# Performance work log

Hardware: AMD Instinct MI355X
Metric: run time of the kernel (lower is better)

Reference implementation:

```python
import jax, jax.numpy as jnp
import numpy as np

N_STEPS = 10
DT = 0.01
TAU = 0.1
LAM = 0.1


def setup_inputs() -> dict:
    key = jax.random.key(0)
    k1, k2 = jax.random.split(key)
    x = jax.random.normal(k1, (4, 2048, 1024), dtype=jnp.float32)
    W = jax.random.normal(k2, (1024, 4096), dtype=jnp.float32) * 0.02
    return {"x": x, "W": W}


def reference(x, W):
    orig_shape = x.shape
    D = orig_shape[-1]
    x_flat = x.reshape(-1, D)                      # [N, d_model]
    b = x_flat @ W                                 # [N, d_lca]
    G = W.T @ W                                    # [d_lca, d_lca]
    G = G - jnp.diag(jnp.diag(G))                  # zero self-inhibition
    u0 = jnp.zeros_like(b)

    def step(u, _):
        a = jax.nn.relu(u - LAM)
        du = (b - a @ G - u) / TAU
        return u + DT * du, None

    u, _ = jax.lax.scan(step, u0, None, length=N_STEPS)
    a = jax.nn.relu(u - LAM)
    out = a @ W.T                                  # [N, d_model]
    return out.reshape(orig_shape)
```

## Files before the change

### kernel.cpp

```cpp
#include <hip/hip_runtime.h>
#include <hip/hip_bf16.h>


typedef __bf16 bf16_t;
typedef __bf16 bf16x8 __attribute__((ext_vector_type(8)));
typedef __bf16 bf16x4 __attribute__((ext_vector_type(4)));
typedef float  f32x4  __attribute__((ext_vector_type(4)));

__device__ __forceinline__ void g2lds16(const void* g, void* l) {
    __builtin_amdgcn_global_load_lds(
        (const __attribute__((address_space(1))) void*)g,
        (__attribute__((address_space(3))) void*)l,
        16, 0, 0);
}

template<int N> __device__ __forceinline__ void waitv() {
    if constexpr (N == 0) asm volatile("s_waitcnt vmcnt(0)" ::: "memory");
    else if constexpr (N == 1) asm volatile("s_waitcnt vmcnt(1)" ::: "memory");
    else if constexpr (N == 2) asm volatile("s_waitcnt vmcnt(2)" ::: "memory");
    else if constexpr (N == 3) asm volatile("s_waitcnt vmcnt(3)" ::: "memory");
    else if constexpr (N == 4) asm volatile("s_waitcnt vmcnt(4)" ::: "memory");
    else if constexpr (N == 5) asm volatile("s_waitcnt vmcnt(5)" ::: "memory");
    else if constexpr (N == 6) asm volatile("s_waitcnt vmcnt(6)" ::: "memory");
}
__device__ __forceinline__ void bar() { __builtin_amdgcn_s_barrier(); }
__device__ __forceinline__ void waitlgkm0() {
    asm volatile("s_waitcnt lgkmcnt(0)" ::: "memory");
}
__device__ __forceinline__ void fence() { asm volatile("" ::: "memory"); }

template<int n> struct IC { static constexpr int v = n; };

enum { MODE_B = 0, MODE_T = 1, MODE_STEP2 = 2, MODE_OUT = 3 };

template<int MODE, int BM>
__global__ __launch_bounds__(512, 2)
void gemm_bt(const bf16_t* __restrict__ A, const bf16_t* __restrict__ Bt,
             int N, int K,
             float*  __restrict__ outF,
             bf16_t* __restrict__ outH,
             bf16_t* __restrict__ bb,
             bf16_t* __restrict__ u,
             const float* __restrict__ g)
{
    constexpr int BN  = 256;
    constexpr int FM  = BM / 32;
    constexpr int FMH = FM / 2;
    constexpr int ASZ = BM * 128;
    constexpr int BSZ = BN * 128;

    __shared__ __attribute__((aligned(16))) bf16_t As[2 * BM * 64];
    __shared__ __attribute__((aligned(16))) bf16_t Bs[2 * BN * 64];

    const int t = threadIdx.x;
    const int l = t & 63;
    const int w = t >> 6;
    const int wm = (w >> 2) * (BM / 4);
    const int wn = (w & 3) * 32;

    const int gx  = gridDim.x;
    const int nwg = gx * gridDim.y;
    const int bid = blockIdx.y * gx + blockIdx.x;
    const int sw  = (bid & 7) * (nwg >> 3) + (bid >> 3);
    const int rowA = (sw / gx) * BM;
    const int colB = (sw % gx) * BN;

    const int srow = t >> 3;
    const int scol = (((t & 7) ^ (srow & 7)) << 3);
    const bf16_t* gB = Bt + (size_t)(colB + srow) * K + scol;
    char* sB = (char*)Bs + t * 16;
    auto stB = [&](int slot, int kt, int uu) {
        g2lds16(gB + (size_t)uu * 64 * K + kt * 64, sB + slot * BSZ + uu * 8192);
    };

    const int lrow = l & 15;
    const int c0 = ((l >> 4) << 4) ^ ((l & 7) << 4);
    const char* cAs = (const char*)As;
    const char* cBs = (const char*)Bs;
    auto rdA = [&](int slot, int qi, int ii, int p) {
        return (const bf16x8*)(cAs + slot * ASZ
            + (size_t)(qi * (BM / 2) + wm + ii * 16 + lrow) * 128 + (c0 ^ (p << 6)));
    };
    auto rdB = [&](int slot, int qj, int jj, int p) {
        return (const bf16x8*)(cBs + slot * BSZ
            + (size_t)(qj * 128 + wn + jj * 16 + lrow) * 128 + (c0 ^ (p << 6)));
    };

    f32x4 acc[FM][4];
#pragma unroll
    for (int i = 0; i < FM; ++i)
#pragma unroll
        for (int j = 0; j < 4; ++j)
#pragma unroll
            for (int r = 0; r < 4; ++r) acc[i][j][r] = 0.f;

    const int NT = K >> 6;

    if constexpr (BM == 256) {
        const bf16_t* gA = A + (size_t)(rowA + srow) * K + scol;
        char* sA = (char*)As + t * 16;
        auto stA = [&](int slot, int kt, int uu) {
            g2lds16(gA + (size_t)uu * 64 * K + kt * 64, sA + slot * ASZ + uu * 8192);
        };

        auto tile = [&](auto W0, auto W1, auto W2, int slot, int ktN, bool st) {
            const int ns = slot ^ 1;
            bf16x8 af[FMH][2], bf0[2][2], bf1[2][2];
            if (st) { stB(ns, ktN, 0); stB(ns, ktN, 1); }
            waitv<decltype(W0)::v>(); bar();
#pragma unroll
            for (int ii = 0; ii < FMH; ++ii)
#pragma unroll
                for (int p = 0; p < 2; ++p) af[ii][p] = *rdA(slot, 0, ii, p);
#pragma unroll
            for (int jj = 0; jj < 2; ++jj)
#pragma unroll
                for (int p = 0; p < 2; ++p) bf0[jj][p] = *rdB(slot, 0, jj, p);
            __builtin_amdgcn_s_setprio(1);
#pragma unroll
            for (int ii = 0; ii < FMH; ++ii)
#pragma unroll
                for (int jj = 0; jj < 2; ++jj)
#pragma unroll
                    for (int p = 0; p < 2; ++p)
                        acc[ii][jj] = __builtin_amdgcn_mfma_f32_16x16x32_bf16(
                            bf0[jj][p], af[ii][p], acc[ii][jj], 0, 0, 0);
            __builtin_amdgcn_s_setprio(0);
            if (st) { stA(ns, ktN, 0); stA(ns, ktN, 1); }
            waitv<decltype(W1)::v>(); bar();
#pragma unroll
            for (int jj = 0; jj < 2; ++jj)
#pragma unroll
                for (int p = 0; p < 2; ++p) bf1[jj][p] = *rdB(slot, 1, jj, p);
            __builtin_amdgcn_s_setprio(1);
#pragma unroll
            for (int ii = 0; ii < FMH; ++ii)
#pragma unroll
                for (int jj = 0; jj < 2; ++jj)
#pragma unroll
                    for (int p = 0; p < 2; ++p)
                        acc[ii][2 + jj] = __builtin_amdgcn_mfma_f32_16x16x32_bf16(
                            bf1[jj][p], af[ii][p], acc[ii][2 + jj], 0, 0, 0);
            __builtin_amdgcn_s_setprio(0);
            if (st) { stB(ns, ktN, 2); stB(ns, ktN, 3); }
            waitv<decltype(W2)::v>(); bar();
#pragma unroll
            for (int ii = 0; ii < FMH; ++ii)
#pragma unroll
                for (int p = 0; p < 2; ++p) af[ii][p] = *rdA(slot, 1, ii, p);
            __builtin_amdgcn_s_setprio(1);
#pragma unroll
            for (int ii = 0; ii < FMH; ++ii)
#pragma unroll
                for (int jj = 0; jj < 2; ++jj)
#pragma unroll
                    for (int p = 0; p < 2; ++p)
                        acc[FMH + ii][2 + jj] = __builtin_amdgcn_mfma_f32_16x16x32_bf16(
                            bf1[jj][p], af[ii][p], acc[FMH + ii][2 + jj], 0, 0, 0);
            __builtin_amdgcn_s_setprio(0);
            if (st) { stA(ns, ktN, 2); stA(ns, ktN, 3); }
            __builtin_amdgcn_s_setprio(1);
#pragma unroll
            for (int ii = 0; ii < FMH; ++ii)
#pragma unroll
                for (int jj = 0; jj < 2; ++jj)
#pragma unroll
                    for (int p = 0; p < 2; ++p)
                        acc[FMH + ii][jj] = __builtin_amdgcn_mfma_f32_16x16x32_bf16(
                            bf0[jj][p], af[ii][p], acc[FMH + ii][jj], 0, 0, 0);
            __builtin_amdgcn_s_setprio(0);
        };

        stB(0, 0, 0); stB(0, 0, 1);
        stA(0, 0, 0); stA(0, 0, 1);
        stB(0, 0, 2); stB(0, 0, 3);
        stA(0, 0, 2); stA(0, 0, 3);

        for (int kt = 0; kt < NT - 1; ++kt)
            tile(IC<6>{}, IC<6>{}, IC<6>{}, kt & 1, kt + 1, true);
        tile(IC<4>{}, IC<2>{}, IC<0>{}, (NT - 1) & 1, 0, false);
    } else {
        const int s_arow = t >> 3;
        const int s_acb  = ((t & 7) << 4) ^ ((s_arow & 7) << 4);
        const bf16_t* gAr = A + (size_t)(rowA + s_arow) * K + (t & 7) * 8;
        auto reluv = [&](bf16x8 v) {
            bf16x8 r;
#pragma unroll
            for (int e = 0; e < 8; ++e)
                r[e] = (bf16_t)fmaxf((float)v[e] - 0.1f, 0.f);
            return r;
        };
        auto wrA = [&](bf16x8 v, int gg, int slot) {
            *(bf16x8*)((char*)As + slot * ASZ
                       + (size_t)(gg * 64 + s_arow) * 128 + s_acb) = v;
        };

        bf16x8 curA0, curA1;
        {
            bf16x8 p0 = *(const bf16x8*)(gAr);
            bf16x8 p1 = *(const bf16x8*)(gAr + (size_t)64 * K);
            waitv<0>();
            wrA(reluv(p0), 0, 0);
            wrA(reluv(p1), 1, 0);
            waitlgkm0();
            curA0 = *(const bf16x8*)(gAr + 64);
            curA1 = *(const bf16x8*)(gAr + (size_t)64 * K + 64);
            fence();
            stB(0, 0, 0); stB(0, 0, 1); stB(0, 0, 2); stB(0, 0, 3);
        }

        for (int kt = 0; kt < NT; ++kt) {
            const int slot = kt & 1, ns = slot ^ 1;
            const bool iA = (kt + 2 < NT);
            const bool sB = (kt + 1 < NT);
            bf16x8 af[FMH][2], bf0[2][2], bf1[2][2];
            bf16x8 nA0, nA1;
            if (iA) {
                nA0 = *(const bf16x8*)(gAr + (kt + 2) * 64);
                nA1 = *(const bf16x8*)(gAr + (size_t)64 * K + (kt + 2) * 64);
            }
            if (kt < NT - 2) waitv<4>(); else waitv<2>();
            bar();
#pragma unroll
            for (int ii = 0; ii < FMH; ++ii)
#pragma unroll
                for (int p = 0; p < 2; ++p) af[ii][p] = *rdA(slot, 0, ii, p);
#pragma unroll
            for (int jj = 0; jj < 2; ++jj)
#pragma unroll
                for (int p = 0; p < 2; ++p) bf0[jj][p] = *rdB(slot, 0, jj, p);
            __builtin_amdgcn_s_setprio(1);
#pragma unroll
            for (int ii = 0; ii < FMH; ++ii)
#pragma unroll
                for (int jj = 0; jj < 2; ++jj)
#pragma unroll
                    for (int p = 0; p < 2; ++p)
                        acc[ii][jj] = __builtin_amdgcn_mfma_f32_16x16x32_bf16(
                            bf0[jj][p], af[ii][p], acc[ii][jj], 0, 0, 0);
            __builtin_amdgcn_s_setprio(0);
            if (sB) { stB(ns, kt + 1, 0); stB(ns, kt + 1, 1); }
            if (kt < NT - 2) waitv<4>();
            else if (kt == NT - 2) waitv<2>();
            else waitv<0>();
            bar();
#pragma unroll
            for (int jj = 0; jj < 2; ++jj)
#pragma unroll
                for (int p = 0; p < 2; ++p) bf1[jj][p] = *rdB(slot, 1, jj, p);
            __builtin_amdgcn_s_setprio(1);
#pragma unroll
            for (int ii = 0; ii < FMH; ++ii)
#pragma unroll
                for (int jj = 0; jj < 2; ++jj)
#pragma unroll
                    for (int p = 0; p < 2; ++p)
                        acc[ii][2 + jj] = __builtin_amdgcn_mfma_f32_16x16x32_bf16(
                            bf1[jj][p], af[ii][p], acc[ii][2 + jj], 0, 0, 0);
            __builtin_amdgcn_s_setprio(0);
            if (sB) { stB(ns, kt + 1, 2); stB(ns, kt + 1, 3); }
#pragma unroll
            for (int ii = 0; ii < FMH; ++ii)
#pragma unroll
                for (int p = 0; p < 2; ++p) af[ii][p] = *rdA(slot, 1, ii, p);
            if (sB) {
                wrA(reluv(curA0), 0, ns);
                wrA(reluv(curA1), 1, ns);
            }
            __builtin_amdgcn_s_setprio(1);
#pragma unroll
            for (int ii = 0; ii < FMH; ++ii)
#pragma unroll
                for (int jj = 0; jj < 2; ++jj)
#pragma unroll
                    for (int p = 0; p < 2; ++p)
                        acc[FMH + ii][2 + jj] = __builtin_amdgcn_mfma_f32_16x16x32_bf16(
                            bf1[jj][p], af[ii][p], acc[FMH + ii][2 + jj], 0, 0, 0);
            __builtin_amdgcn_s_setprio(0);
            waitlgkm0();
            __builtin_amdgcn_s_setprio(1);
#pragma unroll
            for (int ii = 0; ii < FMH; ++ii)
#pragma unroll
                for (int jj = 0; jj < 2; ++jj)
#pragma unroll
                    for (int p = 0; p < 2; ++p)
                        acc[FMH + ii][jj] = __builtin_amdgcn_mfma_f32_16x16x32_bf16(
                            bf0[jj][p], af[ii][p], acc[FMH + ii][jj], 0, 0, 0);
            __builtin_amdgcn_s_setprio(0);
            if (iA) { curA0 = nA0; curA1 = nA1; }
        }
    }

    const int m0 = rowA + wm + lrow;
    const int n0 = colB + wn + ((l >> 4) * 4);

    f32x4 gvv[4];
    if constexpr (MODE == MODE_STEP2) {
#pragma unroll
        for (int j = 0; j < 4; ++j)
            gvv[j] = *(const f32x4*)(g + n0 + (j & 1) * 16 + (j >> 1) * 128);
    }

#pragma unroll
    for (int i = 0; i < FM; ++i) {
        const int m = m0 + (i & (FMH - 1)) * 16 + (i / FMH) * (BM / 2);
#pragma unroll
        for (int j = 0; j < 4; ++j) {
            const size_t idx = (size_t)m * N + (n0 + (j & 1) * 16 + (j >> 1) * 128);
            const f32x4 c = acc[i][j];
            if constexpr (MODE == MODE_T) {
                bf16x4 o;
#pragma unroll
                for (int r = 0; r < 4; ++r) o[r] = (bf16_t)c[r];
                *(bf16x4*)(outH + idx) = o;
            } else if constexpr (MODE == MODE_B) {
                bf16x4 ob, ou;
#pragma unroll
                for (int r = 0; r < 4; ++r) {
                    const float un = 0.1f * c[r];
                    ob[r] = (bf16_t)c[r];
                    ou[r] = (bf16_t)un;
                }
                *(bf16x4*)(bb + idx) = ob;
                *(bf16x4*)(u  + idx) = ou;
            } else if constexpr (MODE == MODE_STEP2) {
                const bf16x4 uv = *(const bf16x4*)(u  + idx);
                const bf16x4 bv = *(const bf16x4*)(bb + idx);
                bf16x4 ou;
#pragma unroll
                for (int r = 0; r < 4; ++r) {
                    const float uo = (float)uv[r];
                    const float ao = fmaxf(uo - 0.1f, 0.f);
                    const float un = 0.9f * uo + 0.1f * (float)bv[r]
                                   - 0.1f * c[r] + 0.1f * ao * gvv[j][r];
                    ou[r] = (bf16_t)un;
                }
                *(bf16x4*)(u + idx) = ou;
            } else {
                *(f32x4*)(outF + idx) = c;
            }
        }
    }
}

__global__ void cast_x_kernel(const float* __restrict__ x, bf16_t* __restrict__ xh, int n) {
    int i = (blockIdx.x * 256 + threadIdx.x) * 4;
    if (i < n) {
        f32x4 v = *(const f32x4*)(x + i);
        bf16x4 o;
#pragma unroll
        for (int r = 0; r < 4; ++r) o[r] = (bf16_t)v[r];
        *(bf16x4*)(xh + i) = o;
    }
}

__global__ void prep_w_kernel(const float* __restrict__ W,
                              bf16_t* __restrict__ Wh, bf16_t* __restrict__ WT) {
    __shared__ bf16_t tile[64][130];
    const int k0 = blockIdx.y * 64;
    const int n0 = blockIdx.x * 128;
    for (int e = threadIdx.x; e < 64 * 128; e += 256) {
        const int kk = e >> 7, nn = e & 127;
        const bf16_t v = (bf16_t)W[(size_t)(k0 + kk) * 4096 + n0 + nn];
        Wh[(size_t)(k0 + kk) * 4096 + n0 + nn] = v;
        tile[kk][nn] = v;
    }
    __syncthreads();
    for (int e = threadIdx.x; e < 64 * 128; e += 256) {
        const int nn = e >> 6, kk = e & 63;
        WT[(size_t)(n0 + nn) * 1024 + k0 + kk] = tile[kk][nn];
    }
}

__global__ void zero_g_kernel(float* __restrict__ g) {
    int i = blockIdx.x * 256 + threadIdx.x;
    if (i < 4096) g[i] = 0.f;
}

__global__ void prep_g_kernel(const float* __restrict__ W, float* __restrict__ g) {
    const int j  = blockIdx.x * 256 + threadIdx.x;
    const int k0 = blockIdx.y * 128;
    float s = 0.f;
    for (int k = k0; k < k0 + 128; ++k) {
        const float v = W[(size_t)k * 4096 + j];
        s += v * v;
    }
    atomicAdd(g + j, s);
}

extern "C" void kernel_launch(void* const* d_in, const int* in_sizes, int n_in,
                              void* d_out, int out_size, void* d_ws, size_t ws_size,
                              hipStream_t stream)
{
    const float* x = (const float*)d_in[0];
    const float* W = (const float*)d_in[1];

    bf16_t* xh = (bf16_t*)d_out;
    bf16_t* tt = (bf16_t*)d_out;
    float*  gd = (float*)((char*)d_out + 16777216);

    char* ws = (char*)d_ws;
    bf16_t* bb = (bf16_t*)(ws + 67108864);
    bf16_t* u  = (bf16_t*)(ws + 134217728);
    bf16_t* Wh = (bf16_t*)(ws + 201326592);
    bf16_t* WT = (bf16_t*)(ws + 209715200);

    cast_x_kernel<<<8388608 / 1024, 256, 0, stream>>>(x, xh, 8388608);
    prep_w_kernel<<<dim3(32, 16), 256, 0, stream>>>(W, Wh, WT);
    zero_g_kernel<<<16, 256, 0, stream>>>(gd);
    prep_g_kernel<<<dim3(16, 8), 256, 0, stream>>>(W, gd);

    gemm_bt<MODE_B, 256><<<dim3(16, 32), 512, 0, stream>>>(xh, WT, 4096, 1024,
                                                           nullptr, nullptr, bb, u, nullptr);
    for (int s = 0; s < 9; ++s) {
        gemm_bt<MODE_T, 128><<<dim3(4, 64), 512, 0, stream>>>(u, Wh, 1024, 4096,
                                                              nullptr, tt, nullptr, nullptr, nullptr);
        gemm_bt<MODE_STEP2, 256><<<dim3(16, 32), 512, 0, stream>>>(tt, WT, 4096, 1024,
                                                                   nullptr, nullptr, bb, u, gd);
    }
    gemm_bt<MODE_OUT, 128><<<dim3(4, 64), 512, 0, stream>>>(u, Wh, 1024, 4096,
                                                            (float*)d_out, nullptr, nullptr, nullptr, nullptr);
}
```

Measured before the change: 1.775 ms.

## Restructure GEMM tile pipelines to drop barriers and prefetch next-tile fragments

```diff
diff --git a/kernel.cpp b/kernel.cpp
--- a/kernel.cpp
+++ b/kernel.cpp
@@ -103,9 +103,24 @@
             g2lds16(gA + (size_t)uu * 64 * K + kt * 64, sA + slot * ASZ + uu * 8192);
         };
 
-        auto tile = [&](auto W0, auto W1, auto W2, int slot, int ktN, bool st) {
+        auto MQ = [&](int qi, int qj, bf16x8 (&Af)[FMH][2], bf16x8 (&Bf)[2][2]) {
+            __builtin_amdgcn_s_setprio(1);
+#pragma unroll
+            for (int ii = 0; ii < FMH; ++ii)
+#pragma unroll
+                for (int jj = 0; jj < 2; ++jj)
+#pragma unroll
+                    for (int p = 0; p < 2; ++p)
+                        acc[qi * FMH + ii][qj * 2 + jj] =
+                            __builtin_amdgcn_mfma_f32_16x16x32_bf16(
+                                Bf[jj][p], Af[ii][p],
+                                acc[qi * FMH + ii][qj * 2 + jj], 0, 0, 0);
+            __builtin_amdgcn_s_setprio(0);
+        };
+
+        auto tile = [&](auto W0, auto W2, int slot, int ktN, bool st) {
             const int ns = slot ^ 1;
-            bf16x8 af[FMH][2], bf0[2][2], bf1[2][2];
+            bf16x8 af[FMH][2], bfA[2][2], bfB[2][2];
             if (st) { stB(ns, ktN, 0); stB(ns, ktN, 1); }
             waitv<decltype(W0)::v>(); bar();
 #pragma unroll
@@ -115,60 +130,23 @@
 #pragma unroll
             for (int jj = 0; jj < 2; ++jj)
 #pragma unroll
-                for (int p = 0; p < 2; ++p) bf0[jj][p] = *rdB(slot, 0, jj, p);
-            __builtin_amdgcn_s_setprio(1);
-#pragma unroll
-            for (int ii = 0; ii < FMH; ++ii)
-#pragma unroll
-                for (int jj = 0; jj < 2; ++jj)
-#pragma unroll
-                    for (int p = 0; p < 2; ++p)
-                        acc[ii][jj] = __builtin_amdgcn_mfma_f32_16x16x32_bf16(
-                            bf0[jj][p], af[ii][p], acc[ii][jj], 0, 0, 0);
-            __builtin_amdgcn_s_setprio(0);
+                for (int p = 0; p < 2; ++p) bfA[jj][p] = *rdB(slot, 0, jj, p);
+#pragma unroll
+            for (int jj = 0; jj < 2; ++jj)
+#pragma unroll
+                for (int p = 0; p < 2; ++p) bfB[jj][p] = *rdB(slot, 1, jj, p);
+            MQ(0, 0, af, bfA);
             if (st) { stA(ns, ktN, 0); stA(ns, ktN, 1); }
-            waitv<decltype(W1)::v>(); bar();
-#pragma unroll
-            for (int jj = 0; jj < 2; ++jj)
-#pragma unroll
-                for (int p = 0; p < 2; ++p) bf1[jj][p] = *rdB(slot, 1, jj, p);
-            __builtin_amdgcn_s_setprio(1);
-#pragma unroll
-            for (int ii = 0; ii < FMH; ++ii)
-#pragma unroll
-                for (int jj = 0; jj < 2; ++jj)
-#pragma unroll
-                    for (int p = 0; p < 2; ++p)
-                        acc[ii][2 + jj] = __builtin_amdgcn_mfma_f32_16x16x32_bf16(
-                            bf1[jj][p], af[ii][p], acc[ii][2 + jj], 0, 0, 0);
-            __builtin_amdgcn_s_setprio(0);
+            MQ(0, 1, af, bfB);
             if (st) { stB(ns, ktN, 2); stB(ns, ktN, 3); }
             waitv<decltype(W2)::v>(); bar();
 #pragma unroll
             for (int ii = 0; ii < FMH; ++ii)
 #pragma unroll
                 for (int p = 0; p < 2; ++p) af[ii][p] = *rdA(slot, 1, ii, p);
-            __builtin_amdgcn_s_setprio(1);
-#pragma unroll
-            for (int ii = 0; ii < FMH; ++ii)
-#pragma unroll
-                for (int jj = 0; jj < 2; ++jj)
-#pragma unroll
-                    for (int p = 0; p < 2; ++p)
-                        acc[FMH + ii][2 + jj] = __builtin_amdgcn_mfma_f32_16x16x32_bf16(
-                            bf1[jj][p], af[ii][p], acc[FMH + ii][2 + jj], 0, 0, 0);
-            __builtin_amdgcn_s_setprio(0);
+            MQ(1, 1, af, bfB);
             if (st) { stA(ns, ktN, 2); stA(ns, ktN, 3); }
-            __builtin_amdgcn_s_setprio(1);
-#pragma unroll
-            for (int ii = 0; ii < FMH; ++ii)
-#pragma unroll
-                for (int jj = 0; jj < 2; ++jj)
-#pragma unroll
-                    for (int p = 0; p < 2; ++p)
-                        acc[FMH + ii][jj] = __builtin_amdgcn_mfma_f32_16x16x32_bf16(
-                            bf0[jj][p], af[ii][p], acc[FMH + ii][jj], 0, 0, 0);
-            __builtin_amdgcn_s_setprio(0);
+            MQ(1, 0, af, bfA);
         };
 
         stB(0, 0, 0); stB(0, 0, 1);
@@ -177,8 +155,8 @@
         stA(0, 0, 2); stA(0, 0, 3);
 
         for (int kt = 0; kt < NT - 1; ++kt)
-            tile(IC<6>{}, IC<6>{}, IC<6>{}, kt & 1, kt + 1, true);
-        tile(IC<4>{}, IC<2>{}, IC<0>{}, (NT - 1) & 1, 0, false);
+            tile(IC<4>{}, IC<4>{}, kt & 1, kt + 1, true);
+        tile(IC<2>{}, IC<0>{}, (NT - 1) & 1, 0, false);
     } else {
         const int s_arow = t >> 3;
         const int s_acb  = ((t & 7) << 4) ^ ((s_arow & 7) << 4);
@@ -195,7 +173,24 @@
                        + (size_t)(gg * 64 + s_arow) * 128 + s_acb) = v;
         };
 
-        bf16x8 curA0, curA1;
+        auto MQ = [&](int qi, int qj, bf16x8 (&Af)[FMH][2], bf16x8 (&Bf)[2][2]) {
+            __builtin_amdgcn_s_setprio(1);
+#pragma unroll
+            for (int ii = 0; ii < FMH; ++ii)
+#pragma unroll
+                for (int jj = 0; jj < 2; ++jj)
+#pragma unroll
+                    for (int p = 0; p < 2; ++p)
+                        acc[qi * FMH + ii][qj * 2 + jj] =
+                            __builtin_amdgcn_mfma_f32_16x16x32_bf16(
+                                Bf[jj][p], Af[ii][p],
+                                acc[qi * FMH + ii][qj * 2 + jj], 0, 0, 0);
+            __builtin_amdgcn_s_setprio(0);
+        };
+
+        bf16x8 af0[FMH][2], af1[FMH][2], bf1v[2][2], bf0A[2][2], bf0B[2][2];
+        bf16x8 curA0, curA1, nA0, nA1;
+
         {
             bf16x8 p0 = *(const bf16x8*)(gAr);
             bf16x8 p1 = *(const bf16x8*)(gAr + (size_t)64 * K);
@@ -207,38 +202,23 @@
             curA1 = *(const bf16x8*)(gAr + (size_t)64 * K + 64);
             fence();
             stB(0, 0, 0); stB(0, 0, 1); stB(0, 0, 2); stB(0, 0, 3);
+            waitv<2>(); bar();
+            nA0 = *(const bf16x8*)(gAr + 2 * 64);
+            nA1 = *(const bf16x8*)(gAr + (size_t)64 * K + 2 * 64);
+            fence();
+#pragma unroll
+            for (int ii = 0; ii < FMH; ++ii)
+#pragma unroll
+                for (int p = 0; p < 2; ++p) af0[ii][p] = *rdA(0, 0, ii, p);
+#pragma unroll
+            for (int jj = 0; jj < 2; ++jj)
+#pragma unroll
+                for (int p = 0; p < 2; ++p) bf0A[jj][p] = *rdB(0, 0, jj, p);
         }
 
-        for (int kt = 0; kt < NT; ++kt) {
+        auto tb = [&](int kt, bf16x8 (&b0c)[2][2], bf16x8 (&b0n)[2][2]) {
             const int slot = kt & 1, ns = slot ^ 1;
-            const bool iA = (kt + 2 < NT);
-            const bool sB = (kt + 1 < NT);
-            bf16x8 af[FMH][2], bf0[2][2], bf1[2][2];
-            bf16x8 nA0, nA1;
-            if (iA) {
-                nA0 = *(const bf16x8*)(gAr + (kt + 2) * 64);
-                nA1 = *(const bf16x8*)(gAr + (size_t)64 * K + (kt + 2) * 64);
-            }
-            if (kt < NT - 2) waitv<4>(); else waitv<2>();
-            bar();
-#pragma unroll
-            for (int ii = 0; ii < FMH; ++ii)
-#pragma unroll
-                for (int p = 0; p < 2; ++p) af[ii][p] = *rdA(slot, 0, ii, p);
-#pragma unroll
-            for (int jj = 0; jj < 2; ++jj)
-#pragma unroll
-                for (int p = 0; p < 2; ++p) bf0[jj][p] = *rdB(slot, 0, jj, p);
-            __builtin_amdgcn_s_setprio(1);
-#pragma unroll
-            for (int ii = 0; ii < FMH; ++ii)
-#pragma unroll
-                for (int jj = 0; jj < 2; ++jj)
-#pragma unroll
-                    for (int p = 0; p < 2; ++p)
-                        acc[ii][jj] = __builtin_amdgcn_mfma_f32_16x16x32_bf16(
-                            bf0[jj][p], af[ii][p], acc[ii][jj], 0, 0, 0);
-            __builtin_amdgcn_s_setprio(0);
+            const bool sB = kt + 1 < NT;
             if (sB) { stB(ns, kt + 1, 0); stB(ns, kt + 1, 1); }
             if (kt < NT - 2) waitv<4>();
             else if (kt == NT - 2) waitv<2>();
@@ -247,48 +227,40 @@
 #pragma unroll
             for (int jj = 0; jj < 2; ++jj)
 #pragma unroll
-                for (int p = 0; p < 2; ++p) bf1[jj][p] = *rdB(slot, 1, jj, p);
-            __builtin_amdgcn_s_setprio(1);
-#pragma unroll
-            for (int ii = 0; ii < FMH; ++ii)
+                for (int p = 0; p < 2; ++p) bf1v[jj][p] = *rdB(slot, 1, jj, p);
+            MQ(0, 0, af0, b0c);
+            if (sB) { stB(ns, kt + 1, 2); stB(ns, kt + 1, 3); }
+#pragma unroll
+            for (int ii = 0; ii < FMH; ++ii)
+#pragma unroll
+                for (int p = 0; p < 2; ++p) af1[ii][p] = *rdA(slot, 1, ii, p);
+            if (sB) { wrA(reluv(curA0), 0, ns); wrA(reluv(curA1), 1, ns); }
+            MQ(0, 1, af0, bf1v);
+            waitlgkm0();
+            MQ(1, 1, af1, bf1v);
+            if (sB) {
+                waitv<2>(); bar();
+                curA0 = nA0; curA1 = nA1;
+                if (kt + 3 < NT) {
+                    nA0 = *(const bf16x8*)(gAr + (size_t)(kt + 3) * 64);
+                    nA1 = *(const bf16x8*)(gAr + (size_t)64 * K + (size_t)(kt + 3) * 64);
+                    fence();
+                }
+#pragma unroll
+                for (int ii = 0; ii < FMH; ++ii)
+#pragma unroll
+                    for (int p = 0; p < 2; ++p) af0[ii][p] = *rdA(ns, 0, ii, p);
 #pragma unroll
                 for (int jj = 0; jj < 2; ++jj)
 #pragma unroll
-                    for (int p = 0; p < 2; ++p)
-                        acc[ii][2 + jj] = __builtin_amdgcn_mfma_f32_16x16x32_bf16(
-                            bf1[jj][p], af[ii][p], acc[ii][2 + jj], 0, 0, 0);
-            __builtin_amdgcn_s_setprio(0);
-            if (sB) { stB(ns, kt + 1, 2); stB(ns, kt + 1, 3); }
-#pragma unroll
-            for (int ii = 0; ii < FMH; ++ii)
-#pragma unroll
-                for (int p = 0; p < 2; ++p) af[ii][p] = *rdA(slot, 1, ii, p);
-            if (sB) {
-                wrA(reluv(curA0), 0, ns);
-                wrA(reluv(curA1), 1, ns);
+                    for (int p = 0; p < 2; ++p) b0n[jj][p] = *rdB(ns, 0, jj, p);
             }
-            __builtin_amdgcn_s_setprio(1);
-#pragma unroll
-            for (int ii = 0; ii < FMH; ++ii)
-#pragma unroll
-                for (int jj = 0; jj < 2; ++jj)
-#pragma unroll
-                    for (int p = 0; p < 2; ++p)
-                        acc[FMH + ii][2 + jj] = __builtin_amdgcn_mfma_f32_16x16x32_bf16(
-                            bf1[jj][p], af[ii][p], acc[FMH + ii][2 + jj], 0, 0, 0);
-            __builtin_amdgcn_s_setprio(0);
-            waitlgkm0();
-            __builtin_amdgcn_s_setprio(1);
-#pragma unroll
-            for (int ii = 0; ii < FMH; ++ii)
-#pragma unroll
-                for (int jj = 0; jj < 2; ++jj)
-#pragma unroll
-                    for (int p = 0; p < 2; ++p)
-                        acc[FMH + ii][jj] = __builtin_amdgcn_mfma_f32_16x16x32_bf16(
-                            bf0[jj][p], af[ii][p], acc[FMH + ii][jj], 0, 0, 0);
-            __builtin_amdgcn_s_setprio(0);
-            if (iA) { curA0 = nA0; curA1 = nA1; }
+            MQ(1, 0, af1, b0c);
+        };
+
+        for (int kt = 0; kt < NT; kt += 2) {
+            tb(kt, bf0A, bf0B);
+            tb(kt + 1, bf0B, bf0A);
         }
     }
 
```

After: 1.715 ms. 3.4% less time.
